# Optimization experiments

Measured on AMD Instinct MI355X. Metric: run time of the kernel, lower is better.

Reference implementation:

```python
import jax, jax.numpy as jnp
import numpy as np

NUM_PAGES = 4096
PAGE_SIZE = 16
KV_HEADS = 8
HEAD_SIZE = 128
N_TOKENS = 8192


def setup_inputs() -> dict:
    key = jax.random.key(0)
    k1, k2, k3, k4, k5 = jax.random.split(key, 5)
    kv_pages = jax.random.normal(k1, (NUM_PAGES, PAGE_SIZE, 2 * KV_HEADS, HEAD_SIZE), dtype=jnp.float32)
    new_k = jax.random.normal(k2, (N_TOKENS, KV_HEADS, HEAD_SIZE), dtype=jnp.float32)
    new_v = jax.random.normal(k3, (N_TOKENS, KV_HEADS, HEAD_SIZE), dtype=jnp.float32)
    t_pages = jax.random.randint(k4, (N_TOKENS,), 0, NUM_PAGES, dtype=jnp.int32)
    t_slots = jax.random.randint(k5, (N_TOKENS,), 0, PAGE_SIZE, dtype=jnp.int32)
    return {"kv_pages": kv_pages, "new_k": new_k, "new_v": new_v,
            "t_pages": t_pages, "t_slots": t_slots}


def reference(kv_pages, new_k, new_v, t_pages, t_slots):
    # Paged KV-cache scatter write: keys go to even kv_head indices, values to odd.
    # mode='drop' matches the haliax .at[...].set(..., mode='drop') semantics
    # (out-of-range page/slot indices are silently dropped).
    new_k = new_k.astype(kv_pages.dtype)
    new_v = new_v.astype(kv_pages.dtype)
    out = kv_pages.at[t_pages, t_slots, 0::2].set(new_k, mode='drop')
    out = out.at[t_pages, t_slots, 1::2].set(new_v, mode='drop')
    return out
```

## Files before the change

kernel.cpp:

```cpp
#include <hip/hip_runtime.h>


#define NUM_PAGES 4096
#define PAGE_SIZE 16
#define KV_HEADS 8
#define HEAD_SIZE 128
#define N_TOKENS 8192
#define NUM_ROWS (NUM_PAGES * PAGE_SIZE)
#define ROW_F4 (2 * KV_HEADS * HEAD_SIZE / 4)
#define ROWS_PER_BLOCK 8

typedef float f32x4 __attribute__((ext_vector_type(4)));

__global__ void kv_winners_kernel(const int* __restrict__ t_pages,
                                  const int* __restrict__ t_slots,
                                  int* __restrict__ winner) {
    int i = blockIdx.x * blockDim.x + threadIdx.x;
    if (i >= N_TOKENS) return;
    int p = t_pages[i];
    int s = t_slots[i];
    if ((unsigned)p < (unsigned)NUM_PAGES && (unsigned)s < (unsigned)PAGE_SIZE) {
        atomicMax(&winner[p * PAGE_SIZE + s], i);
    }
}

__global__ __launch_bounds__(256)
void kv_write_kernel(const f32x4* __restrict__ kv_pages,
                     const float* __restrict__ new_k,
                     const float* __restrict__ new_v,
                     const int* __restrict__ winner,
                     f32x4* __restrict__ out) {
    const int row0 = blockIdx.x * ROWS_PER_BLOCK;

    int w[ROWS_PER_BLOCK];
    #pragma unroll
    for (int r = 0; r < ROWS_PER_BLOCK; ++r) w[r] = winner[row0 + r];

    #pragma unroll
    for (int r = 0; r < ROWS_PER_BLOCK; ++r) {
        const int row = row0 + r;
        const size_t base4 = (size_t)row * ROW_F4;
        if (w[r] < 0) {
            #pragma unroll
            for (int t = threadIdx.x; t < ROW_F4; t += 256) {
                f32x4 v = __builtin_nontemporal_load(&kv_pages[base4 + t]);
                __builtin_nontemporal_store(v, &out[base4 + t]);
            }
        } else {
            const int wi = w[r];
            #pragma unroll
            for (int t = threadIdx.x; t < ROW_F4; t += 256) {
                int head = t >> 5;
                int d4   = t & 31;
                const float* src = (head & 1) ? new_v : new_k;
                size_t off = ((size_t)wi * KV_HEADS + (head >> 1)) * HEAD_SIZE + d4 * 4;
                f32x4 v = *reinterpret_cast<const f32x4*>(src + off);
                __builtin_nontemporal_store(v, &out[base4 + t]);
            }
        }
    }
}

extern "C" void kernel_launch(void* const* d_in, const int* in_sizes, int n_in,
                              void* d_out, int out_size, void* d_ws, size_t ws_size,
                              hipStream_t stream) {
    const float* kv_pages = (const float*)d_in[0];
    const float* new_k    = (const float*)d_in[1];
    const float* new_v    = (const float*)d_in[2];
    const int*   t_pages  = (const int*)d_in[3];
    const int*   t_slots  = (const int*)d_in[4];
    float*       out      = (float*)d_out;
    int*         winner   = (int*)d_ws;

    (void)hipMemsetAsync(winner, 0xFF, NUM_ROWS * sizeof(int), stream);

    kv_winners_kernel<<<(N_TOKENS + 255) / 256, 256, 0, stream>>>(t_pages, t_slots, winner);

    kv_write_kernel<<<NUM_ROWS / ROWS_PER_BLOCK, 256, 0, stream>>>(
        (const f32x4*)kv_pages, new_k, new_v, winner, (f32x4*)out);
}
```

Before: 199.3 us.

## Fuse winner computation into write kernel via per-block LDS token scan

Removes the memset and the separate atomicMax winner kernel. Each block now scans every token index and resolves the last writer for its 8 rows with LDS atomics. The write path also switches the new_k/new_v loads to nontemporal. This saves launches and the global winner array, but every block must redundantly read the full index arrays.

```diff
diff --git a/kernel.cpp b/kernel.cpp
--- a/kernel.cpp
+++ b/kernel.cpp
@@ -12,49 +12,51 @@
 
 typedef float f32x4 __attribute__((ext_vector_type(4)));
 
-__global__ void kv_winners_kernel(const int* __restrict__ t_pages,
-                                  const int* __restrict__ t_slots,
-                                  int* __restrict__ winner) {
-    int i = blockIdx.x * blockDim.x + threadIdx.x;
-    if (i >= N_TOKENS) return;
-    int p = t_pages[i];
-    int s = t_slots[i];
-    if ((unsigned)p < (unsigned)NUM_PAGES && (unsigned)s < (unsigned)PAGE_SIZE) {
-        atomicMax(&winner[p * PAGE_SIZE + s], i);
-    }
-}
-
 __global__ __launch_bounds__(256)
-void kv_write_kernel(const f32x4* __restrict__ kv_pages,
+void kv_fused_kernel(const f32x4* __restrict__ kv_pages,
                      const float* __restrict__ new_k,
                      const float* __restrict__ new_v,
-                     const int* __restrict__ winner,
+                     const int* __restrict__ t_pages,
+                     const int* __restrict__ t_slots,
                      f32x4* __restrict__ out) {
+    __shared__ int wlds[ROWS_PER_BLOCK];
     const int row0 = blockIdx.x * ROWS_PER_BLOCK;
+    const int tid  = threadIdx.x;
 
-    int w[ROWS_PER_BLOCK];
-    #pragma unroll
-    for (int r = 0; r < ROWS_PER_BLOCK; ++r) w[r] = winner[row0 + r];
+    if (tid < ROWS_PER_BLOCK) wlds[tid] = -1;
+    __syncthreads();
+
+    #pragma unroll 4
+    for (int i = tid; i < N_TOKENS; i += 256) {
+        int p = t_pages[i];
+        int s = t_slots[i];
+        if ((unsigned)p < (unsigned)NUM_PAGES && (unsigned)s < (unsigned)PAGE_SIZE) {
+            int d = p * PAGE_SIZE + s - row0;
+            if ((unsigned)d < (unsigned)ROWS_PER_BLOCK)
+                atomicMax(&wlds[d], i);
+        }
+    }
+    __syncthreads();
 
     #pragma unroll
     for (int r = 0; r < ROWS_PER_BLOCK; ++r) {
-        const int row = row0 + r;
-        const size_t base4 = (size_t)row * ROW_F4;
-        if (w[r] < 0) {
+        const int w = wlds[r];
+        const size_t base4 = (size_t)(row0 + r) * ROW_F4;
+        if (w < 0) {
             #pragma unroll
-            for (int t = threadIdx.x; t < ROW_F4; t += 256) {
+            for (int t = tid; t < ROW_F4; t += 256) {
                 f32x4 v = __builtin_nontemporal_load(&kv_pages[base4 + t]);
                 __builtin_nontemporal_store(v, &out[base4 + t]);
             }
         } else {
-            const int wi = w[r];
             #pragma unroll
-            for (int t = threadIdx.x; t < ROW_F4; t += 256) {
+            for (int t = tid; t < ROW_F4; t += 256) {
                 int head = t >> 5;
                 int d4   = t & 31;
                 const float* src = (head & 1) ? new_v : new_k;
-                size_t off = ((size_t)wi * KV_HEADS + (head >> 1)) * HEAD_SIZE + d4 * 4;
-                f32x4 v = *reinterpret_cast<const f32x4*>(src + off);
+                size_t off = ((size_t)w * KV_HEADS + (head >> 1)) * HEAD_SIZE + d4 * 4;
+                f32x4 v = __builtin_nontemporal_load(
+                    reinterpret_cast<const f32x4*>(src + off));
                 __builtin_nontemporal_store(v, &out[base4 + t]);
             }
         }
@@ -70,12 +72,7 @@
     const int*   t_pages  = (const int*)d_in[3];
     const int*   t_slots  = (const int*)d_in[4];
     float*       out      = (float*)d_out;
-    int*         winner   = (int*)d_ws;
 
-    (void)hipMemsetAsync(winner, 0xFF, NUM_ROWS * sizeof(int), stream);
-
-    kv_winners_kernel<<<(N_TOKENS + 255) / 256, 256, 0, stream>>>(t_pages, t_slots, winner);
-
-    kv_write_kernel<<<NUM_ROWS / ROWS_PER_BLOCK, 256, 0, stream>>>(
-        (const f32x4*)kv_pages, new_k, new_v, winner, (f32x4*)out);
+    kv_fused_kernel<<<NUM_ROWS / ROWS_PER_BLOCK, 256, 0, stream>>>(
+        (const f32x4*)kv_pages, new_k, new_v, t_pages, t_slots, (f32x4*)out);
 }
```

Result: slower. 221.3 us (+11.0%).
